# Optimization experiments

Measured on AMD Instinct MI355X. Metric: run time of the kernel, lower is better.

## Reference

```python
import jax, jax.numpy as jnp
import numpy as np

B, N, D = 64, 512, 256
IMG = 51  # hard-coded image-token prefix length from the original forward
EPS = 1e-8


def _l2norm(x):
    # matches torch.cosine_similarity eps clamping on each vector norm
    n = jnp.linalg.norm(x, axis=-1, keepdims=True)
    return x / jnp.maximum(n, EPS)


def setup_inputs() -> dict:
    key = jax.random.key(0)
    ks = jax.random.split(key, 10)
    s = 1.0 / np.sqrt(D)
    return {
        "input_1": jax.random.normal(ks[0], (B, N, D), jnp.float32),
        "input_2": jax.random.normal(ks[1], (B, N, D), jnp.float32),
        "attention_mask": jnp.ones((B, N), jnp.int32),  # unused by forward, kept for signature fidelity
        "noun_mask": jax.random.randint(ks[2], (B, N), 0, 2, jnp.int32),
        "w0": jax.random.uniform(ks[3], (D, D), jnp.float32, -s, s),
        "b0": jax.random.uniform(ks[4], (D,), jnp.float32, -s, s),
        "w1": jax.random.uniform(ks[5], (D, D), jnp.float32, -s, s),
        "b1": jax.random.uniform(ks[6], (D,), jnp.float32, -s, s),
        "wf": jax.random.uniform(ks[7], (D, D), jnp.float32, -s, s),
        "bf": jax.random.uniform(ks[8], (D,), jnp.float32, -s, s),
    }


def reference(input_1, input_2, attention_mask, noun_mask, w0, b0, w1, b1, wf, bf):
    img = _l2norm(input_2[:, :IMG, :])    # [B, 51, D]
    text = _l2norm(input_2[:, IMG:, :])   # [B, N-51, D]
    # cosine similarity via normalized matmul (no O(N*M*D) repeat blowup)
    sim = jnp.einsum('bid,btd->bit', img, text)            # [B, 51, N-51]
    nm = noun_mask[:, IMG:].astype(sim.dtype)[:, None, :]  # [B, 1, N-51]
    sim = sim * nm
    text_sim = jnp.einsum('bid,bjd->bij', text, text)      # [B, N-51, N-51]
    adj = jnp.zeros((B, N, N), input_2.dtype)
    adj = adj.at[:, :IMG, IMG:].set(sim)
    adj = adj.at[:, IMG:, :IMG].set(jnp.swapaxes(sim, 1, 2))
    adj = adj.at[:, IMG:, IMG:].set(text_sim)
    h = input_1
    for w, b in ((w0, b0), (w1, b1)):  # gcn_layer_num = 2; dropout is identity at eval
        h = jax.nn.relu(jnp.einsum('bnm,bmd->bnd', adj, h) @ w.T + b)
    return jax.nn.relu(h @ wf.T + bf)
```

## Files before the change

### kernel.cpp

```cpp
#include <hip/hip_runtime.h>
#include <math.h>

#define Bn   64
#define Nn   512
#define Dn   256
#define IMGn 51

typedef __attribute__((ext_vector_type(8))) short bf16x8;
typedef __attribute__((ext_vector_type(4))) float f32x4;
typedef __attribute__((ext_vector_type(4))) unsigned short u16x4;

__device__ inline unsigned short f2b(float f) {
    union { float f; unsigned u; } v; v.f = f;
    unsigned r = v.u + 0x7fffu + ((v.u >> 16) & 1u);
    return (unsigned short)(r >> 16);
}

__global__ __launch_bounds__(256) void k_prep(const float* __restrict__ in1,
                                              const float* __restrict__ in2,
                                              const float* __restrict__ w0,
                                              const float* __restrict__ w1,
                                              const float* __restrict__ wf,
                                              unsigned short* __restrict__ A0,
                                              unsigned short* __restrict__ T,
                                              unsigned short* __restrict__ w0b,
                                              unsigned short* __restrict__ w1b,
                                              unsigned short* __restrict__ wfb) {
    const int bid = blockIdx.x, tid = threadIdx.x;
    if (bid < 8192) {
        const int row = bid * 4 + (tid >> 6);
        const int lane = tid & 63;
        float4 v = ((const float4*)(in2 + (size_t)row * Dn))[lane];
        float ss = v.x * v.x + v.y * v.y + v.z * v.z + v.w * v.w;
#pragma unroll
        for (int m = 1; m < 64; m <<= 1) ss += __shfl_xor(ss, m);
        float inv = 1.0f / fmaxf(sqrtf(ss), 1e-8f);
        u16x4 o = { f2b(v.x*inv), f2b(v.y*inv), f2b(v.z*inv), f2b(v.w*inv) };
        ((u16x4*)(T + (size_t)row * Dn))[lane] = o;
    } else if (bid < 10240) {
        int i = (bid - 8192) * 256 + tid;
#pragma unroll
        for (int q = 0; q < 4; ++q, i += 524288) {
            float4 v = ((const float4*)in1)[i];
            u16x4 o = { f2b(v.x), f2b(v.y), f2b(v.z), f2b(v.w) };
            ((u16x4*)A0)[i] = o;
        }
    } else {
        const int b2 = bid - 10240;
        const float* src = (b2 < 64) ? w0 : (b2 < 128) ? w1 : wf;
        unsigned short* dst = (b2 < 64) ? w0b : (b2 < 128) ? w1b : wfb;
        const int i = (b2 & 63) * 256 + tid;
        float4 v = ((const float4*)src)[i];
        u16x4 o = { f2b(v.x), f2b(v.y), f2b(v.z), f2b(v.w) };
        ((u16x4*)dst)[i] = o;
    }
}


__device__ inline void stage128x32(const unsigned short* __restrict__ src, int ldk,
                                   char* ldsbase, int tid) {
    const int wave = tid >> 6, lane = tid & 63;
#pragma unroll
    for (int it = 0; it < 2; ++it) {
        const int chunk = wave * 128 + it * 64 + lane;
        const int row = chunk >> 2, s = chunk & 3;
        const char* g = (const char*)(src + (size_t)row * ldk) + ((s ^ ((row >> 1) & 3)) << 4);
        char* l = ldsbase + (size_t)(wave * 2048 + it * 1024);
        __builtin_amdgcn_global_load_lds((const __attribute__((address_space(1))) void*)g,
                                         (__attribute__((address_space(3))) void*)l,
                                         16, 0, 0);
    }
}

__device__ inline bf16x8 frag(const char* ldsbase, int row, int s) {
    return *(const bf16x8*)(ldsbase + row * 64 + ((s ^ ((row >> 1) & 3)) << 4));
}

enum { EPI_GRAM = 0, EPI_TRANS = 1, EPI_BIASH = 2, EPI_FINAL = 3 };

template<int EPI, int NBUF>
__global__ __launch_bounds__(256) void k_mfma(const unsigned short* __restrict__ Abase,
                                              const unsigned short* __restrict__ Bbase,
                                              void* __restrict__ outp,
                                              const float* __restrict__ bias,
                                              const int* __restrict__ noun,
                                              int K, int lda, int ldb, long sA, long sB) {
    extern __shared__ char smem[];
    const int tid = threadIdx.x, lane = tid & 63, wave = tid >> 6;
    const int wr = wave >> 1, wc = wave & 1;
    const int r16 = lane & 15, s = lane >> 4;
    (void)lane;

    const int nwg = gridDim.x * gridDim.y * gridDim.z;
    const int wg  = blockIdx.x + gridDim.x * (blockIdx.y + gridDim.y * blockIdx.z);
    const int swz = (wg & 7) * (nwg >> 3) + (wg >> 3);
    const int tile_x = swz % gridDim.x;
    const int rem    = swz / gridDim.x;
    const int tile_y = rem % gridDim.y;
    const size_t bz  = rem / gridDim.y;

    const unsigned short* A  = Abase + bz * sA + (size_t)tile_y * 128 * lda;
    const unsigned short* Bt = Bbase + bz * sB + (size_t)tile_x * 128 * ldb;

    f32x4 acc[4][4];
#pragma unroll
    for (int m = 0; m < 4; ++m)
#pragma unroll
        for (int n = 0; n < 4; ++n)
            acc[m][n] = (f32x4){0.f, 0.f, 0.f, 0.f};

    const int NT = K >> 5;

    if constexpr (NBUF == 2) {
        stage128x32(A,  lda, smem,        tid);
        stage128x32(Bt, ldb, smem + 8192, tid);
        for (int t = 0; t < NT; ++t) {
            asm volatile("s_waitcnt vmcnt(0)" ::: "memory");
            __builtin_amdgcn_s_barrier();
            __builtin_amdgcn_sched_barrier(0);
            if (t + 1 < NT) {
                char* nb = smem + 16384 * ((t + 1) & 1);
                stage128x32(A  + (t + 1) * 32, lda, nb,        tid);
                stage128x32(Bt + (t + 1) * 32, ldb, nb + 8192, tid);
            }
            __builtin_amdgcn_sched_barrier(0);
            const char* cb = smem + 16384 * (t & 1);
            bf16x8 af[4], bv[4];
#pragma unroll
            for (int m = 0; m < 4; ++m) af[m] = frag(cb, wr * 64 + m * 16 + r16, s);
#pragma unroll
            for (int n = 0; n < 4; ++n) bv[n] = frag(cb + 8192, wc * 64 + n * 16 + r16, s);
#pragma unroll
            for (int m = 0; m < 4; ++m)
#pragma unroll
                for (int n = 0; n < 4; ++n)
                    acc[m][n] = __builtin_amdgcn_mfma_f32_16x16x32_bf16(af[m], bv[n], acc[m][n], 0, 0, 0);
        }
    } else {
        stage128x32(A,       lda, smem,                tid);
        stage128x32(Bt,      ldb, smem + 8192,         tid);
        stage128x32(A + 32,  lda, smem + 16384,        tid);
        stage128x32(Bt + 32, ldb, smem + 16384 + 8192, tid);
        for (int t = 0; t < NT; ++t) {
            if (t < NT - 1) { asm volatile("s_waitcnt vmcnt(4)" ::: "memory"); }
            else            { asm volatile("s_waitcnt vmcnt(0)" ::: "memory"); }
            __builtin_amdgcn_s_barrier();
            __builtin_amdgcn_sched_barrier(0);
            if (t + 2 < NT) {
                char* nb = smem + 16384 * ((t + 2) % 3);
                stage128x32(A  + (t + 2) * 32, lda, nb,        tid);
                stage128x32(Bt + (t + 2) * 32, ldb, nb + 8192, tid);
            }
            __builtin_amdgcn_sched_barrier(0);
            const char* cb = smem + 16384 * (t % 3);
            bf16x8 af[4], bv[4];
#pragma unroll
            for (int m = 0; m < 4; ++m) af[m] = frag(cb, wr * 64 + m * 16 + r16, s);
#pragma unroll
            for (int n = 0; n < 4; ++n) bv[n] = frag(cb + 8192, wc * 64 + n * 16 + r16, s);
#pragma unroll
            for (int m = 0; m < 4; ++m)
#pragma unroll
                for (int n = 0; n < 4; ++n)
                    acc[m][n] = __builtin_amdgcn_mfma_f32_16x16x32_bf16(af[m], bv[n], acc[m][n], 0, 0, 0);
        }
    }
    __syncthreads();

    const int row0 = tile_y * 128, col0 = tile_x * 128;
    unsigned short* lt = (unsigned short*)smem;
    const int row = tid >> 1, h = tid & 1;

    if constexpr (EPI == EPI_GRAM) {
        const int* nm = noun + bz * Nn;
        unsigned short* out = (unsigned short*)outp + bz * ((size_t)Nn * Nn);
#pragma unroll
        for (int n = 0; n < 4; ++n) {
            const int cl = wc * 64 + n * 16 + r16;
            const int c  = col0 + cl;
            const float nmc = (c < IMGn) ? 0.f : (float)nm[c];
#pragma unroll
            for (int m = 0; m < 4; ++m)
#pragma unroll
                for (int i = 0; i < 4; ++i) {
                    const int rl = wr * 64 + m * 16 + s * 4 + i;
                    const int r  = row0 + rl;
                    float mask;
                    if (r < IMGn)      mask = nmc;
                    else if (c < IMGn) mask = (float)nm[r];
                    else               mask = 1.f;
                    lt[rl * 136 + cl] = f2b(acc[m][n][i] * mask);
                }
        }
        __syncthreads();
        const bf16x8* srcv = (const bf16x8*)(lt + (size_t)row * 136 + h * 64);
        bf16x8* dstv = (bf16x8*)(out + (size_t)(row0 + row) * Nn + col0 + h * 64);
#pragma unroll
        for (int q = 0; q < 8; ++q) dstv[q] = srcv[q];
    } else if constexpr (EPI == EPI_BIASH) {
#pragma unroll
        for (int n = 0; n < 4; ++n) {
            const int cl = wc * 64 + n * 16 + r16;
            const float bvv = bias[col0 + cl];
#pragma unroll
            for (int m = 0; m < 4; ++m)
#pragma unroll
                for (int i = 0; i < 4; ++i) {
                    const int rl = wr * 64 + m * 16 + s * 4 + i;
                    lt[rl * 136 + cl] = f2b(fmaxf(acc[m][n][i] + bvv, 0.f));
                }
        }
        __syncthreads();
        unsigned short* out = (unsigned short*)outp + bz * ((size_t)Nn * Dn);
        const bf16x8* srcv = (const bf16x8*)(lt + (size_t)row * 136 + h * 64);
        bf16x8* dstv = (bf16x8*)(out + (size_t)(row0 + row) * Dn + col0 + h * 64);
#pragma unroll
        for (int q = 0; q < 8; ++q) dstv[q] = srcv[q];
    } else if constexpr (EPI == EPI_FINAL) {
        float* lt32 = (float*)smem;
        float* out = (float*)outp;
#pragma unroll
        for (int p = 0; p < 2; ++p) {
            if (p) __syncthreads();
            if (wc == p) {
#pragma unroll
                for (int n = 0; n < 4; ++n) {
                    const int cll = n * 16 + r16;
                    const float bvv = bias[col0 + p * 64 + cll];
#pragma unroll
                    for (int m = 0; m < 4; ++m)
#pragma unroll
                        for (int i = 0; i < 4; ++i) {
                            const int rl = wr * 64 + m * 16 + s * 4 + i;
                            lt32[rl * 68 + cll] = fmaxf(acc[m][n][i] + bvv, 0.f);
                        }
                }
            }
            __syncthreads();
            const float4* srcv = (const float4*)(lt32 + (size_t)row * 68 + h * 32);
            float4* dstv = (float4*)(out + (size_t)(row0 + row) * Dn + col0 + p * 64 + h * 32);
#pragma unroll
            for (int q = 0; q < 8; ++q) dstv[q] = srcv[q];
        }
    } else {
#pragma unroll
        for (int n = 0; n < 4; ++n)
#pragma unroll
            for (int m = 0; m < 4; ++m)
#pragma unroll
                for (int i = 0; i < 4; ++i) {
                    const int ct = wc * 64 + n * 16 + r16;
                    const int rt = wr * 64 + m * 16 + s * 4 + i;
                    lt[ct * 136 + rt] = f2b(acc[m][n][i]);
                }
        __syncthreads();
        const int bm = tile_y;
        const size_t bb = bm >> 2;
        const int rl0 = (bm & 3) * 128;
        unsigned short* out = (unsigned short*)outp + bb * ((size_t)Dn * Nn);
        const int ct = tid >> 1;
        const bf16x8* srcv = (const bf16x8*)(lt + (size_t)ct * 136 + h * 64);
        bf16x8* dstv = (bf16x8*)(out + (size_t)(col0 + ct) * Nn + rl0 + h * 64);
#pragma unroll
        for (int q = 0; q < 8; ++q) dstv[q] = srcv[q];
    }
}

extern "C" void kernel_launch(void* const* d_in, const int* in_sizes, int n_in,
                              void* d_out, int out_size, void* d_ws, size_t ws_size,
                              hipStream_t stream) {
    const float* input_1 = (const float*)d_in[0];
    const float* input_2 = (const float*)d_in[1];
    const int*   noun    = (const int*)d_in[3];
    const float* w0 = (const float*)d_in[4];
    const float* b0 = (const float*)d_in[5];
    const float* w1 = (const float*)d_in[6];
    const float* b1 = (const float*)d_in[7];
    const float* wf = (const float*)d_in[8];
    const float* bf = (const float*)d_in[9];

    unsigned short* ws  = (unsigned short*)d_ws;
    unsigned short* T   = ws;
    unsigned short* A0  = ws + 8388608;
    unsigned short* adj = ws + 16777216;
    unsigned short* Ut  = ws + 33554432;
    unsigned short* H1  = ws + 41943040;
    unsigned short* H2  = ws + 50331648;
    unsigned short* w0b = ws + 58720256;
    unsigned short* w1b = w0b + 65536;
    unsigned short* wfb = w1b + 65536;

    dim3 blk(256);
    k_prep<<<10432, blk, 0, stream>>>(input_1, input_2, w0, w1, wf, A0, T, w0b, w1b, wfb);

    k_mfma<EPI_GRAM, 2><<<dim3(4, 4, Bn), blk, 34816, stream>>>(
        T, T, adj, nullptr, noun, 256, 256, 256, (long)Nn * Dn, (long)Nn * Dn);
    k_mfma<EPI_TRANS, 3><<<dim3(2, 256, 1), blk, 49152, stream>>>(
        A0, w0b, Ut, nullptr, nullptr, 256, 256, 256, 0, 0);
    k_mfma<EPI_BIASH, 3><<<dim3(2, 4, Bn), blk, 49152, stream>>>(
        adj, Ut, H1, b0, nullptr, 512, 512, 512, (long)Nn * Nn, (long)Dn * Nn);
    k_mfma<EPI_TRANS, 3><<<dim3(2, 256, 1), blk, 49152, stream>>>(
        H1, w1b, Ut, nullptr, nullptr, 256, 256, 256, 0, 0);
    k_mfma<EPI_BIASH, 3><<<dim3(2, 4, Bn), blk, 49152, stream>>>(
        adj, Ut, H2, b1, nullptr, 512, 512, 512, (long)Nn * Nn, (long)Dn * Nn);
    k_mfma<EPI_FINAL, 3><<<dim3(2, 256, 1), blk, 49152, stream>>>(
        H2, wfb, d_out, bf, nullptr, 256, 256, 256, 0, 0);
}
```

Measured before the change: 140.5 us.

## Fuse Gram adjacency computation into aggregation matmul, drop materialized adj

The separate Gram kernel that wrote the masked 512x512 bf16 adjacency to global memory is removed. Each aggregation block now recomputes its 128x128 adjacency tile from the normalized features, masks it into LDS, and immediately multiplies it by Ut. This removes the adjacency write and its two reads, but the Gram matmul now runs twice (once per GCN layer) and redundantly per output column tile. The fused kernel also uses a larger static LDS footprint with a 2-stage buffer, which may limit occupancy.

```diff
diff --git a/kernel.cpp b/kernel.cpp
--- a/kernel.cpp
+++ b/kernel.cpp
@@ -56,7 +56,6 @@
     }
 }
 
-
 __device__ inline void stage128x32(const unsigned short* __restrict__ src, int ldk,
                                    char* ldsbase, int tid) {
     const int wave = tid >> 6, lane = tid & 63;
@@ -76,20 +75,162 @@
     return *(const bf16x8*)(ldsbase + row * 64 + ((s ^ ((row >> 1) & 3)) << 4));
 }
 
-enum { EPI_GRAM = 0, EPI_TRANS = 1, EPI_BIASH = 2, EPI_FINAL = 3 };
-
-template<int EPI, int NBUF>
+__global__ __launch_bounds__(256, 2) void k_fused(const unsigned short* __restrict__ T_,
+                                                  const unsigned short* __restrict__ Ut,
+                                                  const float* __restrict__ bias,
+                                                  const int* __restrict__ noun,
+                                                  unsigned short* __restrict__ H) {
+    __shared__ char smem[67584];
+    unsigned short* Sbuf = (unsigned short*)(smem + 32768);
+    const int tid = threadIdx.x, lane = tid & 63, wave = tid >> 6;
+    const int wr = wave >> 1, wc = wave & 1;
+    const int r16 = lane & 15, s = lane >> 4;
+
+    const int nwg = gridDim.x * gridDim.y * gridDim.z;
+    const int wg  = blockIdx.x + gridDim.x * (blockIdx.y + gridDim.y * blockIdx.z);
+    const int swz = (wg & 7) * (nwg >> 3) + (wg >> 3);
+    const int c0  = swz % gridDim.x;
+    const int rem = swz / gridDim.x;
+    const int ty  = rem % gridDim.y;
+    const size_t bz = rem / gridDim.y;
+
+    const unsigned short* Tb = T_ + bz * (size_t)(Nn * Dn);
+    const unsigned short* Ar = Tb + (size_t)ty * 128 * Dn;
+    const unsigned short* Ub = Ut + bz * (size_t)(Dn * Nn) + (size_t)c0 * 128 * Nn;
+    const int* nm = noun + bz * Nn;
+
+    f32x4 acc[4][4];
+#pragma unroll
+    for (int m = 0; m < 4; ++m)
+#pragma unroll
+        for (int n = 0; n < 4; ++n) acc[m][n] = (f32x4){0.f, 0.f, 0.f, 0.f};
+
+    stage128x32(Ar, Dn, smem,        tid);
+    stage128x32(Tb, Dn, smem + 8192, tid);
+    int gs = 0;
+
+    for (int ct = 0; ct < 4; ++ct) {
+        const unsigned short* Bp = Tb + (size_t)ct * 128 * Dn;
+        f32x4 sacc[4][4];
+#pragma unroll
+        for (int m = 0; m < 4; ++m)
+#pragma unroll
+            for (int n = 0; n < 4; ++n) sacc[m][n] = (f32x4){0.f, 0.f, 0.f, 0.f};
+
+        for (int j = 0; j < 8; ++j) {
+            asm volatile("s_waitcnt vmcnt(0)" ::: "memory");
+            __builtin_amdgcn_s_barrier();
+            __builtin_amdgcn_sched_barrier(0);
+            char* nb = smem + 16384 * ((gs + 1) & 1);
+            if (j < 7) {
+                stage128x32(Ar + (j + 1) * 32, Dn, nb,        tid);
+                stage128x32(Bp + (j + 1) * 32, Dn, nb + 8192, tid);
+            } else {
+                stage128x32(Ub + ct * 128,      Nn, nb,        tid);
+                stage128x32(Ub + ct * 128 + 32, Nn, nb + 8192, tid);
+            }
+            __builtin_amdgcn_sched_barrier(0);
+            const char* cb = smem + 16384 * (gs & 1);
+            bf16x8 af[4], bv[4];
+#pragma unroll
+            for (int m = 0; m < 4; ++m) af[m] = frag(cb,        wr * 64 + m * 16 + r16, s);
+#pragma unroll
+            for (int n = 0; n < 4; ++n) bv[n] = frag(cb + 8192, wc * 64 + n * 16 + r16, s);
+#pragma unroll
+            for (int m = 0; m < 4; ++m)
+#pragma unroll
+                for (int n = 0; n < 4; ++n)
+                    sacc[m][n] = __builtin_amdgcn_mfma_f32_16x16x32_bf16(af[m], bv[n], sacc[m][n], 0, 0, 0);
+            ++gs;
+        }
+#pragma unroll
+        for (int n = 0; n < 4; ++n) {
+            const int cl = wc * 64 + n * 16 + r16;
+            const int c  = ct * 128 + cl;
+            const float nmc = (c < IMGn) ? 0.f : (float)nm[c];
+#pragma unroll
+            for (int m = 0; m < 4; ++m)
+#pragma unroll
+                for (int i = 0; i < 4; ++i) {
+                    const int rl = wr * 64 + m * 16 + s * 4 + i;
+                    const int r  = ty * 128 + rl;
+                    float mask;
+                    if (r < IMGn)      mask = nmc;
+                    else if (c < IMGn) mask = (float)nm[r];
+                    else               mask = 1.f;
+                    Sbuf[rl * 136 + cl] = f2b(sacc[m][n][i] * mask);
+                }
+        }
+        __syncthreads();
+
+        for (int u = 0; u < 2; ++u) {
+            asm volatile("s_waitcnt vmcnt(0)" ::: "memory");
+            __builtin_amdgcn_s_barrier();
+            __builtin_amdgcn_sched_barrier(0);
+            char* nb = smem + 16384 * ((gs + 1) & 1);
+            if (u == 0) {
+                stage128x32(Ub + ct * 128 + 64, Nn, nb,        tid);
+                stage128x32(Ub + ct * 128 + 96, Nn, nb + 8192, tid);
+            } else if (ct < 3) {
+                stage128x32(Ar,                      Dn, nb,        tid);
+                stage128x32(Tb + (ct + 1) * 128 * Dn, Dn, nb + 8192, tid);
+            }
+            __builtin_amdgcn_sched_barrier(0);
+            const char* cb = smem + 16384 * (gs & 1);
+#pragma unroll
+            for (int h = 0; h < 2; ++h) {
+                const int kk = u * 2 + h;
+                bf16x8 af[4], bv[4];
+#pragma unroll
+                for (int m = 0; m < 4; ++m)
+                    af[m] = *(const bf16x8*)((const char*)Sbuf +
+                              (size_t)(wr * 64 + m * 16 + r16) * 272 + kk * 64 + s * 16);
+#pragma unroll
+                for (int n = 0; n < 4; ++n) bv[n] = frag(cb + h * 8192, wc * 64 + n * 16 + r16, s);
+#pragma unroll
+                for (int m = 0; m < 4; ++m)
+#pragma unroll
+                    for (int n = 0; n < 4; ++n)
+                        acc[m][n] = __builtin_amdgcn_mfma_f32_16x16x32_bf16(af[m], bv[n], acc[m][n], 0, 0, 0);
+            }
+            ++gs;
+        }
+    }
+
+    __syncthreads();
+#pragma unroll
+    for (int n = 0; n < 4; ++n) {
+        const int cl = wc * 64 + n * 16 + r16;
+        const float bvv = bias[c0 * 128 + cl];
+#pragma unroll
+        for (int m = 0; m < 4; ++m)
+#pragma unroll
+            for (int i = 0; i < 4; ++i) {
+                const int rl = wr * 64 + m * 16 + s * 4 + i;
+                Sbuf[rl * 136 + cl] = f2b(fmaxf(acc[m][n][i] + bvv, 0.f));
+            }
+    }
+    __syncthreads();
+    const int row = tid >> 1, h = tid & 1;
+    unsigned short* out = H + bz * (size_t)(Nn * Dn);
+    const bf16x8* srcv = (const bf16x8*)(Sbuf + (size_t)row * 136 + h * 64);
+    bf16x8* dstv = (bf16x8*)(out + (size_t)(ty * 128 + row) * Dn + c0 * 128 + h * 64);
+#pragma unroll
+    for (int q = 0; q < 8; ++q) dstv[q] = srcv[q];
+}
+
+enum { EPI_TRANS = 1, EPI_FINAL = 3 };
+
+template<int EPI>
 __global__ __launch_bounds__(256) void k_mfma(const unsigned short* __restrict__ Abase,
                                               const unsigned short* __restrict__ Bbase,
                                               void* __restrict__ outp,
                                               const float* __restrict__ bias,
-                                              const int* __restrict__ noun,
-                                              int K, int lda, int ldb, long sA, long sB) {
+                                              int K, int lda, int ldb) {
     extern __shared__ char smem[];
     const int tid = threadIdx.x, lane = tid & 63, wave = tid >> 6;
     const int wr = wave >> 1, wc = wave & 1;
     const int r16 = lane & 15, s = lane >> 4;
-    (void)lane;
 
     const int nwg = gridDim.x * gridDim.y * gridDim.z;
     const int wg  = blockIdx.x + gridDim.x * (blockIdx.y + gridDim.y * blockIdx.z);
@@ -97,73 +238,43 @@
     const int tile_x = swz % gridDim.x;
     const int rem    = swz / gridDim.x;
     const int tile_y = rem % gridDim.y;
-    const size_t bz  = rem / gridDim.y;
-
-    const unsigned short* A  = Abase + bz * sA + (size_t)tile_y * 128 * lda;
-    const unsigned short* Bt = Bbase + bz * sB + (size_t)tile_x * 128 * ldb;
+
+    const unsigned short* A  = Abase + (size_t)tile_y * 128 * lda;
+    const unsigned short* Bt = Bbase + (size_t)tile_x * 128 * ldb;
 
     f32x4 acc[4][4];
 #pragma unroll
     for (int m = 0; m < 4; ++m)
 #pragma unroll
-        for (int n = 0; n < 4; ++n)
-            acc[m][n] = (f32x4){0.f, 0.f, 0.f, 0.f};
+        for (int n = 0; n < 4; ++n) acc[m][n] = (f32x4){0.f, 0.f, 0.f, 0.f};
 
     const int NT = K >> 5;
-
-    if constexpr (NBUF == 2) {
-        stage128x32(A,  lda, smem,        tid);
-        stage128x32(Bt, ldb, smem + 8192, tid);
-        for (int t = 0; t < NT; ++t) {
-            asm volatile("s_waitcnt vmcnt(0)" ::: "memory");
-            __builtin_amdgcn_s_barrier();
-            __builtin_amdgcn_sched_barrier(0);
-            if (t + 1 < NT) {
-                char* nb = smem + 16384 * ((t + 1) & 1);
-                stage128x32(A  + (t + 1) * 32, lda, nb,        tid);
-                stage128x32(Bt + (t + 1) * 32, ldb, nb + 8192, tid);
-            }
-            __builtin_amdgcn_sched_barrier(0);
-            const char* cb = smem + 16384 * (t & 1);
-            bf16x8 af[4], bv[4];
-#pragma unroll
-            for (int m = 0; m < 4; ++m) af[m] = frag(cb, wr * 64 + m * 16 + r16, s);
-#pragma unroll
-            for (int n = 0; n < 4; ++n) bv[n] = frag(cb + 8192, wc * 64 + n * 16 + r16, s);
-#pragma unroll
-            for (int m = 0; m < 4; ++m)
-#pragma unroll
-                for (int n = 0; n < 4; ++n)
-                    acc[m][n] = __builtin_amdgcn_mfma_f32_16x16x32_bf16(af[m], bv[n], acc[m][n], 0, 0, 0);
-        }
-    } else {
-        stage128x32(A,       lda, smem,                tid);
-        stage128x32(Bt,      ldb, smem + 8192,         tid);
-        stage128x32(A + 32,  lda, smem + 16384,        tid);
-        stage128x32(Bt + 32, ldb, smem + 16384 + 8192, tid);
-        for (int t = 0; t < NT; ++t) {
-            if (t < NT - 1) { asm volatile("s_waitcnt vmcnt(4)" ::: "memory"); }
-            else            { asm volatile("s_waitcnt vmcnt(0)" ::: "memory"); }
-            __builtin_amdgcn_s_barrier();
-            __builtin_amdgcn_sched_barrier(0);
-            if (t + 2 < NT) {
-                char* nb = smem + 16384 * ((t + 2) % 3);
-                stage128x32(A  + (t + 2) * 32, lda, nb,        tid);
-                stage128x32(Bt + (t + 2) * 32, ldb, nb + 8192, tid);
-            }
-            __builtin_amdgcn_sched_barrier(0);
-            const char* cb = smem + 16384 * (t % 3);
-            bf16x8 af[4], bv[4];
-#pragma unroll
-            for (int m = 0; m < 4; ++m) af[m] = frag(cb, wr * 64 + m * 16 + r16, s);
-#pragma unroll
-            for (int n = 0; n < 4; ++n) bv[n] = frag(cb + 8192, wc * 64 + n * 16 + r16, s);
-#pragma unroll
-            for (int m = 0; m < 4; ++m)
-#pragma unroll
-                for (int n = 0; n < 4; ++n)
-                    acc[m][n] = __builtin_amdgcn_mfma_f32_16x16x32_bf16(af[m], bv[n], acc[m][n], 0, 0, 0);
-        }
+    stage128x32(A,       lda, smem,                tid);
+    stage128x32(Bt,      ldb, smem + 8192,         tid);
+    stage128x32(A + 32,  lda, smem + 16384,        tid);
+    stage128x32(Bt + 32, ldb, smem + 16384 + 8192, tid);
+    for (int t = 0; t < NT; ++t) {
+        if (t < NT - 1) { asm volatile("s_waitcnt vmcnt(4)" ::: "memory"); }
+        else            { asm volatile("s_waitcnt vmcnt(0)" ::: "memory"); }
+        __builtin_amdgcn_s_barrier();
+        __builtin_amdgcn_sched_barrier(0);
+        if (t + 2 < NT) {
+            char* nb = smem + 16384 * ((t + 2) % 3);
+            stage128x32(A  + (t + 2) * 32, lda, nb,        tid);
+            stage128x32(Bt + (t + 2) * 32, ldb, nb + 8192, tid);
+        }
+        __builtin_amdgcn_sched_barrier(0);
+        const char* cb = smem + 16384 * (t % 3);
+        bf16x8 af[4], bv[4];
+#pragma unroll
+        for (int m = 0; m < 4; ++m) af[m] = frag(cb,        wr * 64 + m * 16 + r16, s);
+#pragma unroll
+        for (int n = 0; n < 4; ++n) bv[n] = frag(cb + 8192, wc * 64 + n * 16 + r16, s);
+#pragma unroll
+        for (int m = 0; m < 4; ++m)
+#pragma unroll
+            for (int n = 0; n < 4; ++n)
+                acc[m][n] = __builtin_amdgcn_mfma_f32_16x16x32_bf16(af[m], bv[n], acc[m][n], 0, 0, 0);
     }
     __syncthreads();
 
@@ -171,52 +282,7 @@
     unsigned short* lt = (unsigned short*)smem;
     const int row = tid >> 1, h = tid & 1;
 
-    if constexpr (EPI == EPI_GRAM) {
-        const int* nm = noun + bz * Nn;
-        unsigned short* out = (unsigned short*)outp + bz * ((size_t)Nn * Nn);
-#pragma unroll
-        for (int n = 0; n < 4; ++n) {
-            const int cl = wc * 64 + n * 16 + r16;
-            const int c  = col0 + cl;
-            const float nmc = (c < IMGn) ? 0.f : (float)nm[c];
-#pragma unroll
-            for (int m = 0; m < 4; ++m)
-#pragma unroll
-                for (int i = 0; i < 4; ++i) {
-                    const int rl = wr * 64 + m * 16 + s * 4 + i;
-                    const int r  = row0 + rl;
-                    float mask;
-                    if (r < IMGn)      mask = nmc;
-                    else if (c < IMGn) mask = (float)nm[r];
-                    else               mask = 1.f;
-                    lt[rl * 136 + cl] = f2b(acc[m][n][i] * mask);
-                }
-        }
-        __syncthreads();
-        const bf16x8* srcv = (const bf16x8*)(lt + (size_t)row * 136 + h * 64);
-        bf16x8* dstv = (bf16x8*)(out + (size_t)(row0 + row) * Nn + col0 + h * 64);
-#pragma unroll
-        for (int q = 0; q < 8; ++q) dstv[q] = srcv[q];
-    } else if constexpr (EPI == EPI_BIASH) {
-#pragma unroll
-        for (int n = 0; n < 4; ++n) {
-            const int cl = wc * 64 + n * 16 + r16;
-            const float bvv = bias[col0 + cl];
-#pragma unroll
-            for (int m = 0; m < 4; ++m)
-#pragma unroll
-                for (int i = 0; i < 4; ++i) {
-                    const int rl = wr * 64 + m * 16 + s * 4 + i;
-                    lt[rl * 136 + cl] = f2b(fmaxf(acc[m][n][i] + bvv, 0.f));
-                }
-        }
-        __syncthreads();
-        unsigned short* out = (unsigned short*)outp + bz * ((size_t)Nn * Dn);
-        const bf16x8* srcv = (const bf16x8*)(lt + (size_t)row * 136 + h * 64);
-        bf16x8* dstv = (bf16x8*)(out + (size_t)(row0 + row) * Dn + col0 + h * 64);
-#pragma unroll
-        for (int q = 0; q < 8; ++q) dstv[q] = srcv[q];
-    } else if constexpr (EPI == EPI_FINAL) {
+    if constexpr (EPI == EPI_FINAL) {
         float* lt32 = (float*)smem;
         float* out = (float*)outp;
 #pragma unroll
@@ -258,9 +324,9 @@
         const size_t bb = bm >> 2;
         const int rl0 = (bm & 3) * 128;
         unsigned short* out = (unsigned short*)outp + bb * ((size_t)Dn * Nn);
-        const int ct = tid >> 1;
-        const bf16x8* srcv = (const bf16x8*)(lt + (size_t)ct * 136 + h * 64);
-        bf16x8* dstv = (bf16x8*)(out + (size_t)(col0 + ct) * Nn + rl0 + h * 64);
+        const int ctc = tid >> 1;
+        const bf16x8* srcv = (const bf16x8*)(lt + (size_t)ctc * 136 + h * 64);
+        bf16x8* dstv = (bf16x8*)(out + (size_t)(col0 + ctc) * Nn + rl0 + h * 64);
 #pragma unroll
         for (int q = 0; q < 8; ++q) dstv[q] = srcv[q];
     }
@@ -281,28 +347,23 @@
 
     unsigned short* ws  = (unsigned short*)d_ws;
     unsigned short* T   = ws;
-    unsigned short* A0  = ws + 8388608;
-    unsigned short* adj = ws + 16777216;
-    unsigned short* Ut  = ws + 33554432;
-    unsigned short* H1  = ws + 41943040;
-    unsigned short* H2  = ws + 50331648;
-    unsigned short* w0b = ws + 58720256;
+    unsigned short* A0  = ws +  8388608;
+    unsigned short* Ut  = ws + 16777216;
+    unsigned short* H1  = ws + 25165824;
+    unsigned short* H2  = ws + 33554432;
+    unsigned short* w0b = ws + 41943040;
     unsigned short* w1b = w0b + 65536;
     unsigned short* wfb = w1b + 65536;
 
     dim3 blk(256);
     k_prep<<<10432, blk, 0, stream>>>(input_1, input_2, w0, w1, wf, A0, T, w0b, w1b, wfb);
 
-    k_mfma<EPI_GRAM, 2><<<dim3(4, 4, Bn), blk, 34816, stream>>>(
-        T, T, adj, nullptr, noun, 256, 256, 256, (long)Nn * Dn, (long)Nn * Dn);
-    k_mfma<EPI_TRANS, 3><<<dim3(2, 256, 1), blk, 49152, stream>>>(
-        A0, w0b, Ut, nullptr, nullptr, 256, 256, 256, 0, 0);
-    k_mfma<EPI_BIASH, 3><<<dim3(2, 4, Bn), blk, 49152, stream>>>(
-        adj, Ut, H1, b0, nullptr, 512, 512, 512, (long)Nn * Nn, (long)Dn * Nn);
-    k_mfma<EPI_TRANS, 3><<<dim3(2, 256, 1), blk, 49152, stream>>>(
-        H1, w1b, Ut, nullptr, nullptr, 256, 256, 256, 0, 0);
-    k_mfma<EPI_BIASH, 3><<<dim3(2, 4, Bn), blk, 49152, stream>>>(
-        adj, Ut, H2, b1, nullptr, 512, 512, 512, (long)Nn * Nn, (long)Dn * Nn);
-    k_mfma<EPI_FINAL, 3><<<dim3(2, 256, 1), blk, 49152, stream>>>(
-        H2, wfb, d_out, bf, nullptr, 256, 256, 256, 0, 0);
-}
+    k_mfma<EPI_TRANS><<<dim3(2, 256, 1), blk, 49152, stream>>>(
+        A0, w0b, Ut, nullptr, 256, 256, 256);
+    k_fused<<<dim3(2, 4, Bn), blk, 0, stream>>>(T, Ut, b0, noun, H1);
+    k_mfma<EPI_TRANS><<<dim3(2, 256, 1), blk, 49152, stream>>>(
+        H1, w1b, Ut, nullptr, 256, 256, 256);
+    k_fused<<<dim3(2, 4, Bn), blk, 0, stream>>>(T, Ut, b1, noun, H2);
+    k_mfma<EPI_FINAL><<<dim3(2, 256, 1), blk, 49152, stream>>>(
+        H2, wfb, d_out, bf, 256, 256, 256);
+}
```

Result: slower. 166.7 us (+18.6%).

## Split GEMM template into per-stage kernels with XCD-aware tile mapping and fusion

Applied to the files above, without the earlier changes.

Replaces the generic templated MFMA kernel with dedicated kernels. Block indices are mapped so that each XCD works on a contiguous set of batches, which is meant to keep per-XCD L2 locality from the prep stage through the following GEMMs. The Gram kernel and the first input-times-weight transform are merged into a single launch to cut one launch and its tail. The GEMM loop drops to plain double buffering with __syncthreads, padded LDS buffers and static 34 KB shared memory with a 4-blocks-per-CU launch bound. The trade-off is a simpler pipeline (loads are no longer staged two ahead), possible extra register pressure, and extra barrier overhead.

```diff
diff --git a/kernel.cpp b/kernel.cpp
--- a/kernel.cpp
+++ b/kernel.cpp
@@ -28,7 +28,9 @@
                                               unsigned short* __restrict__ wfb) {
     const int bid = blockIdx.x, tid = threadIdx.x;
     if (bid < 8192) {
-        const int row = bid * 4 + (tid >> 6);
+        const int xcd = bid & 7, j = bid >> 3;
+        const int b = xcd * 8 + (j >> 7), rb = j & 127;
+        const int row = b * 512 + rb * 4 + (tid >> 6);
         const int lane = tid & 63;
         float4 v = ((const float4*)(in2 + (size_t)row * Dn))[lane];
         float ss = v.x * v.x + v.y * v.y + v.z * v.z + v.w * v.w;
@@ -38,9 +40,12 @@
         u16x4 o = { f2b(v.x*inv), f2b(v.y*inv), f2b(v.z*inv), f2b(v.w*inv) };
         ((u16x4*)(T + (size_t)row * Dn))[lane] = o;
     } else if (bid < 10240) {
-        int i = (bid - 8192) * 256 + tid;
-#pragma unroll
-        for (int q = 0; q < 4; ++q, i += 524288) {
+        const int id2 = bid - 8192;
+        const int xcd = id2 & 7, j = id2 >> 3;
+        const int b = xcd * 8 + (j >> 5), jj = j & 31;
+        int i = b * 32768 + jj * 1024 + tid;
+#pragma unroll
+        for (int q = 0; q < 4; ++q, i += 256) {
             float4 v = ((const float4*)in1)[i];
             u16x4 o = { f2b(v.x), f2b(v.y), f2b(v.z), f2b(v.w) };
             ((u16x4*)A0)[i] = o;
@@ -56,7 +61,6 @@
     }
 }
 
-
 __device__ inline void stage128x32(const unsigned short* __restrict__ src, int ldk,
                                    char* ldsbase, int tid) {
     const int wave = tid >> 6, lane = tid & 63;
@@ -76,104 +80,60 @@
     return *(const bf16x8*)(ldsbase + row * 64 + ((s ^ ((row >> 1) & 3)) << 4));
 }
 
-enum { EPI_GRAM = 0, EPI_TRANS = 1, EPI_BIASH = 2, EPI_FINAL = 3 };
-
-template<int EPI, int NBUF>
-__global__ __launch_bounds__(256) void k_mfma(const unsigned short* __restrict__ Abase,
-                                              const unsigned short* __restrict__ Bbase,
-                                              void* __restrict__ outp,
-                                              const float* __restrict__ bias,
-                                              const int* __restrict__ noun,
-                                              int K, int lda, int ldb, long sA, long sB) {
-    extern __shared__ char smem[];
+__device__ inline void gemm_loop(const unsigned short* __restrict__ A,
+                                 const unsigned short* __restrict__ Bt,
+                                 int lda, int ldb, int NT, char* smem, int tid,
+                                 int wr, int wc, int r16, int s, f32x4 (&acc)[4][4]) {
+#pragma unroll
+    for (int m = 0; m < 4; ++m)
+#pragma unroll
+        for (int n = 0; n < 4; ++n) acc[m][n] = (f32x4){0.f, 0.f, 0.f, 0.f};
+    stage128x32(A,  lda, smem,        tid);
+    stage128x32(Bt, ldb, smem + 8192, tid);
+    __syncthreads();
+    for (int t = 0; t < NT; ++t) {
+        if (t + 1 < NT) {
+            char* nb = smem + 17408 * ((t + 1) & 1);
+            stage128x32(A  + (t + 1) * 32, lda, nb,        tid);
+            stage128x32(Bt + (t + 1) * 32, ldb, nb + 8192, tid);
+        }
+        const char* cb = smem + 17408 * (t & 1);
+        bf16x8 af[4], bv[4];
+#pragma unroll
+        for (int m = 0; m < 4; ++m) af[m] = frag(cb,        wr * 64 + m * 16 + r16, s);
+#pragma unroll
+        for (int n = 0; n < 4; ++n) bv[n] = frag(cb + 8192, wc * 64 + n * 16 + r16, s);
+#pragma unroll
+        for (int m = 0; m < 4; ++m)
+#pragma unroll
+            for (int n = 0; n < 4; ++n)
+                acc[m][n] = __builtin_amdgcn_mfma_f32_16x16x32_bf16(af[m], bv[n], acc[m][n], 0, 0, 0);
+        __syncthreads();
+    }
+}
+
+__global__ __launch_bounds__(256, 4) void k_gt(const unsigned short* __restrict__ T_,
+                                               const unsigned short* __restrict__ A0,
+                                               const unsigned short* __restrict__ w0b,
+                                               const int* __restrict__ noun,
+                                               unsigned short* __restrict__ adj,
+                                               unsigned short* __restrict__ Ut) {
+    __shared__ char smem[34816];
     const int tid = threadIdx.x, lane = tid & 63, wave = tid >> 6;
     const int wr = wave >> 1, wc = wave & 1;
     const int r16 = lane & 15, s = lane >> 4;
-    (void)lane;
-
-    const int nwg = gridDim.x * gridDim.y * gridDim.z;
-    const int wg  = blockIdx.x + gridDim.x * (blockIdx.y + gridDim.y * blockIdx.z);
-    const int swz = (wg & 7) * (nwg >> 3) + (wg >> 3);
-    const int tile_x = swz % gridDim.x;
-    const int rem    = swz / gridDim.x;
-    const int tile_y = rem % gridDim.y;
-    const size_t bz  = rem / gridDim.y;
-
-    const unsigned short* A  = Abase + bz * sA + (size_t)tile_y * 128 * lda;
-    const unsigned short* Bt = Bbase + bz * sB + (size_t)tile_x * 128 * ldb;
-
+    const int id = blockIdx.x, xcd = id & 7, gid = id >> 3;
     f32x4 acc[4][4];
-#pragma unroll
-    for (int m = 0; m < 4; ++m)
-#pragma unroll
-        for (int n = 0; n < 4; ++n)
-            acc[m][n] = (f32x4){0.f, 0.f, 0.f, 0.f};
-
-    const int NT = K >> 5;
-
-    if constexpr (NBUF == 2) {
-        stage128x32(A,  lda, smem,        tid);
-        stage128x32(Bt, ldb, smem + 8192, tid);
-        for (int t = 0; t < NT; ++t) {
-            asm volatile("s_waitcnt vmcnt(0)" ::: "memory");
-            __builtin_amdgcn_s_barrier();
-            __builtin_amdgcn_sched_barrier(0);
-            if (t + 1 < NT) {
-                char* nb = smem + 16384 * ((t + 1) & 1);
-                stage128x32(A  + (t + 1) * 32, lda, nb,        tid);
-                stage128x32(Bt + (t + 1) * 32, ldb, nb + 8192, tid);
-            }
-            __builtin_amdgcn_sched_barrier(0);
-            const char* cb = smem + 16384 * (t & 1);
-            bf16x8 af[4], bv[4];
-#pragma unroll
-            for (int m = 0; m < 4; ++m) af[m] = frag(cb, wr * 64 + m * 16 + r16, s);
-#pragma unroll
-            for (int n = 0; n < 4; ++n) bv[n] = frag(cb + 8192, wc * 64 + n * 16 + r16, s);
-#pragma unroll
-            for (int m = 0; m < 4; ++m)
-#pragma unroll
-                for (int n = 0; n < 4; ++n)
-                    acc[m][n] = __builtin_amdgcn_mfma_f32_16x16x32_bf16(af[m], bv[n], acc[m][n], 0, 0, 0);
-        }
-    } else {
-        stage128x32(A,       lda, smem,                tid);
-        stage128x32(Bt,      ldb, smem + 8192,         tid);
-        stage128x32(A + 32,  lda, smem + 16384,        tid);
-        stage128x32(Bt + 32, ldb, smem + 16384 + 8192, tid);
-        for (int t = 0; t < NT; ++t) {
-            if (t < NT - 1) { asm volatile("s_waitcnt vmcnt(4)" ::: "memory"); }
-            else            { asm volatile("s_waitcnt vmcnt(0)" ::: "memory"); }
-            __builtin_amdgcn_s_barrier();
-            __builtin_amdgcn_sched_barrier(0);
-            if (t + 2 < NT) {
-                char* nb = smem + 16384 * ((t + 2) % 3);
-                stage128x32(A  + (t + 2) * 32, lda, nb,        tid);
-                stage128x32(Bt + (t + 2) * 32, ldb, nb + 8192, tid);
-            }
-            __builtin_amdgcn_sched_barrier(0);
-            const char* cb = smem + 16384 * (t % 3);
-            bf16x8 af[4], bv[4];
-#pragma unroll
-            for (int m = 0; m < 4; ++m) af[m] = frag(cb, wr * 64 + m * 16 + r16, s);
-#pragma unroll
-            for (int n = 0; n < 4; ++n) bv[n] = frag(cb + 8192, wc * 64 + n * 16 + r16, s);
-#pragma unroll
-            for (int m = 0; m < 4; ++m)
-#pragma unroll
-                for (int n = 0; n < 4; ++n)
-                    acc[m][n] = __builtin_amdgcn_mfma_f32_16x16x32_bf16(af[m], bv[n], acc[m][n], 0, 0, 0);
-        }
-    }
-    __syncthreads();
-
-    const int row0 = tile_y * 128, col0 = tile_x * 128;
-    unsigned short* lt = (unsigned short*)smem;
-    const int row = tid >> 1, h = tid & 1;
-
-    if constexpr (EPI == EPI_GRAM) {
-        const int* nm = noun + bz * Nn;
-        unsigned short* out = (unsigned short*)outp + bz * ((size_t)Nn * Nn);
+
+    if (gid < 128) {
+        const int b = xcd * 8 + (gid >> 4);
+        const int tile = gid & 15, bx = tile & 3, by = tile >> 2;
+        const unsigned short* Tb = T_ + (size_t)b * Nn * Dn;
+        gemm_loop(Tb + (size_t)by * 128 * Dn, Tb + (size_t)bx * 128 * Dn,
+                  Dn, Dn, 8, smem, tid, wr, wc, r16, s, acc);
+        const int row0 = by * 128, col0 = bx * 128;
+        const int* nm = noun + b * Nn;
+        unsigned short* lt = (unsigned short*)smem;
 #pragma unroll
         for (int n = 0; n < 4; ++n) {
             const int cl = wc * 64 + n * 16 + r16;
@@ -193,56 +153,18 @@
                 }
         }
         __syncthreads();
+        unsigned short* out = adj + (size_t)b * Nn * Nn;
+        const int row = tid >> 1, h = tid & 1;
         const bf16x8* srcv = (const bf16x8*)(lt + (size_t)row * 136 + h * 64);
         bf16x8* dstv = (bf16x8*)(out + (size_t)(row0 + row) * Nn + col0 + h * 64);
 #pragma unroll
         for (int q = 0; q < 8; ++q) dstv[q] = srcv[q];
-    } else if constexpr (EPI == EPI_BIASH) {
-#pragma unroll
-        for (int n = 0; n < 4; ++n) {
-            const int cl = wc * 64 + n * 16 + r16;
-            const float bvv = bias[col0 + cl];
-#pragma unroll
-            for (int m = 0; m < 4; ++m)
-#pragma unroll
-                for (int i = 0; i < 4; ++i) {
-                    const int rl = wr * 64 + m * 16 + s * 4 + i;
-                    lt[rl * 136 + cl] = f2b(fmaxf(acc[m][n][i] + bvv, 0.f));
-                }
-        }
-        __syncthreads();
-        unsigned short* out = (unsigned short*)outp + bz * ((size_t)Nn * Dn);
-        const bf16x8* srcv = (const bf16x8*)(lt + (size_t)row * 136 + h * 64);
-        bf16x8* dstv = (bf16x8*)(out + (size_t)(row0 + row) * Dn + col0 + h * 64);
-#pragma unroll
-        for (int q = 0; q < 8; ++q) dstv[q] = srcv[q];
-    } else if constexpr (EPI == EPI_FINAL) {
-        float* lt32 = (float*)smem;
-        float* out = (float*)outp;
-#pragma unroll
-        for (int p = 0; p < 2; ++p) {
-            if (p) __syncthreads();
-            if (wc == p) {
-#pragma unroll
-                for (int n = 0; n < 4; ++n) {
-                    const int cll = n * 16 + r16;
-                    const float bvv = bias[col0 + p * 64 + cll];
-#pragma unroll
-                    for (int m = 0; m < 4; ++m)
-#pragma unroll
-                        for (int i = 0; i < 4; ++i) {
-                            const int rl = wr * 64 + m * 16 + s * 4 + i;
-                            lt32[rl * 68 + cll] = fmaxf(acc[m][n][i] + bvv, 0.f);
-                        }
-                }
-            }
-            __syncthreads();
-            const float4* srcv = (const float4*)(lt32 + (size_t)row * 68 + h * 32);
-            float4* dstv = (float4*)(out + (size_t)(row0 + row) * Dn + col0 + p * 64 + h * 32);
-#pragma unroll
-            for (int q = 0; q < 8; ++q) dstv[q] = srcv[q];
-        }
     } else {
+        const int idx = xcd * 64 + (gid - 128);
+        const int tx = idx & 1, ty = idx >> 1;
+        gemm_loop(A0 + (size_t)ty * 128 * Dn, w0b + (size_t)tx * 128 * Dn,
+                  Dn, Dn, 8, smem, tid, wr, wc, r16, s, acc);
+        unsigned short* lt = (unsigned short*)smem;
 #pragma unroll
         for (int n = 0; n < 4; ++n)
 #pragma unroll
@@ -254,13 +176,127 @@
                     lt[ct * 136 + rt] = f2b(acc[m][n][i]);
                 }
         __syncthreads();
-        const int bm = tile_y;
-        const size_t bb = bm >> 2;
-        const int rl0 = (bm & 3) * 128;
-        unsigned short* out = (unsigned short*)outp + bb * ((size_t)Dn * Nn);
-        const int ct = tid >> 1;
+        const size_t bb = ty >> 2;
+        const int rl0 = (ty & 3) * 128, col0 = tx * 128;
+        unsigned short* out = Ut + bb * ((size_t)Dn * Nn);
+        const int ct = tid >> 1, h = tid & 1;
         const bf16x8* srcv = (const bf16x8*)(lt + (size_t)ct * 136 + h * 64);
         bf16x8* dstv = (bf16x8*)(out + (size_t)(col0 + ct) * Nn + rl0 + h * 64);
+#pragma unroll
+        for (int q = 0; q < 8; ++q) dstv[q] = srcv[q];
+    }
+}
+
+__global__ __launch_bounds__(256, 4) void k_biash(const unsigned short* __restrict__ adj,
+                                                  const unsigned short* __restrict__ Ut,
+                                                  const float* __restrict__ bias,
+                                                  unsigned short* __restrict__ H) {
+    __shared__ char smem[34816];
+    const int tid = threadIdx.x, lane = tid & 63, wave = tid >> 6;
+    const int wr = wave >> 1, wc = wave & 1;
+    const int r16 = lane & 15, s = lane >> 4;
+    const int id = blockIdx.x, xcd = id & 7, gid = id >> 3;
+    const int b = xcd * 8 + (gid >> 3);
+    const int tile = gid & 7, tx = tile & 1, ty = tile >> 1;
+    f32x4 acc[4][4];
+    gemm_loop(adj + (size_t)b * Nn * Nn + (size_t)ty * 128 * Nn,
+              Ut  + (size_t)b * Dn * Nn + (size_t)tx * 128 * Nn,
+              Nn, Nn, 16, smem, tid, wr, wc, r16, s, acc);
+    const int row0 = ty * 128, col0 = tx * 128;
+    unsigned short* lt = (unsigned short*)smem;
+#pragma unroll
+    for (int n = 0; n < 4; ++n) {
+        const int cl = wc * 64 + n * 16 + r16;
+        const float bvv = bias[col0 + cl];
+#pragma unroll
+        for (int m = 0; m < 4; ++m)
+#pragma unroll
+            for (int i = 0; i < 4; ++i) {
+                const int rl = wr * 64 + m * 16 + s * 4 + i;
+                lt[rl * 136 + cl] = f2b(fmaxf(acc[m][n][i] + bvv, 0.f));
+            }
+    }
+    __syncthreads();
+    unsigned short* out = H + (size_t)b * Nn * Dn;
+    const int row = tid >> 1, h = tid & 1;
+    const bf16x8* srcv = (const bf16x8*)(lt + (size_t)row * 136 + h * 64);
+    bf16x8* dstv = (bf16x8*)(out + (size_t)(row0 + row) * Dn + col0 + h * 64);
+#pragma unroll
+    for (int q = 0; q < 8; ++q) dstv[q] = srcv[q];
+}
+
+__global__ __launch_bounds__(256, 4) void k_trans(const unsigned short* __restrict__ Hin,
+                                                  const unsigned short* __restrict__ Wb,
+                                                  unsigned short* __restrict__ Ut) {
+    __shared__ char smem[34816];
+    const int tid = threadIdx.x, lane = tid & 63, wave = tid >> 6;
+    const int wr = wave >> 1, wc = wave & 1;
+    const int r16 = lane & 15, s = lane >> 4;
+    const int id = blockIdx.x, xcd = id & 7;
+    const int idx = xcd * 64 + (id >> 3);
+    const int tx = idx & 1, ty = idx >> 1;
+    f32x4 acc[4][4];
+    gemm_loop(Hin + (size_t)ty * 128 * Dn, Wb + (size_t)tx * 128 * Dn,
+              Dn, Dn, 8, smem, tid, wr, wc, r16, s, acc);
+    unsigned short* lt = (unsigned short*)smem;
+#pragma unroll
+    for (int n = 0; n < 4; ++n)
+#pragma unroll
+        for (int m = 0; m < 4; ++m)
+#pragma unroll
+            for (int i = 0; i < 4; ++i) {
+                const int ct = wc * 64 + n * 16 + r16;
+                const int rt = wr * 64 + m * 16 + s * 4 + i;
+                lt[ct * 136 + rt] = f2b(acc[m][n][i]);
+            }
+    __syncthreads();
+    const size_t bb = ty >> 2;
+    const int rl0 = (ty & 3) * 128, col0 = tx * 128;
+    unsigned short* out = Ut + bb * ((size_t)Dn * Nn);
+    const int ct = tid >> 1, h = tid & 1;
+    const bf16x8* srcv = (const bf16x8*)(lt + (size_t)ct * 136 + h * 64);
+    bf16x8* dstv = (bf16x8*)(out + (size_t)(col0 + ct) * Nn + rl0 + h * 64);
+#pragma unroll
+    for (int q = 0; q < 8; ++q) dstv[q] = srcv[q];
+}
+
+__global__ __launch_bounds__(256, 4) void k_final(const unsigned short* __restrict__ H2,
+                                                  const unsigned short* __restrict__ wfb,
+                                                  const float* __restrict__ bias,
+                                                  float* __restrict__ out) {
+    __shared__ char smem[34816];
+    const int tid = threadIdx.x, lane = tid & 63, wave = tid >> 6;
+    const int wr = wave >> 1, wc = wave & 1;
+    const int r16 = lane & 15, s = lane >> 4;
+    const int id = blockIdx.x, xcd = id & 7;
+    const int idx = xcd * 64 + (id >> 3);
+    const int tx = idx & 1, ty = idx >> 1;
+    f32x4 acc[4][4];
+    gemm_loop(H2 + (size_t)ty * 128 * Dn, wfb + (size_t)tx * 128 * Dn,
+              Dn, Dn, 8, smem, tid, wr, wc, r16, s, acc);
+    const int row0 = ty * 128, col0 = tx * 128;
+    float* lt32 = (float*)smem;
+    const int row = tid >> 1, h = tid & 1;
+#pragma unroll
+    for (int p = 0; p < 2; ++p) {
+        if (p) __syncthreads();
+        if (wc == p) {
+#pragma unroll
+            for (int n = 0; n < 4; ++n) {
+                const int cll = n * 16 + r16;
+                const float bvv = bias[col0 + p * 64 + cll];
+#pragma unroll
+                for (int m = 0; m < 4; ++m)
+#pragma unroll
+                    for (int i = 0; i < 4; ++i) {
+                        const int rl = wr * 64 + m * 16 + s * 4 + i;
+                        lt32[rl * 68 + cll] = fmaxf(acc[m][n][i] + bvv, 0.f);
+                    }
+            }
+        }
+        __syncthreads();
+        const float4* srcv = (const float4*)(lt32 + (size_t)row * 68 + h * 32);
+        float4* dstv = (float4*)(out + (size_t)(row0 + row) * Dn + col0 + p * 64 + h * 32);
 #pragma unroll
         for (int q = 0; q < 8; ++q) dstv[q] = srcv[q];
     }
@@ -281,7 +317,7 @@
 
     unsigned short* ws  = (unsigned short*)d_ws;
     unsigned short* T   = ws;
-    unsigned short* A0  = ws + 8388608;
+    unsigned short* A0  = ws +  8388608;
     unsigned short* adj = ws + 16777216;
     unsigned short* Ut  = ws + 33554432;
     unsigned short* H1  = ws + 41943040;
@@ -292,17 +328,9 @@
 
     dim3 blk(256);
     k_prep<<<10432, blk, 0, stream>>>(input_1, input_2, w0, w1, wf, A0, T, w0b, w1b, wfb);
-
-    k_mfma<EPI_GRAM, 2><<<dim3(4, 4, Bn), blk, 34816, stream>>>(
-        T, T, adj, nullptr, noun, 256, 256, 256, (long)Nn * Dn, (long)Nn * Dn);
-    k_mfma<EPI_TRANS, 3><<<dim3(2, 256, 1), blk, 49152, stream>>>(
-        A0, w0b, Ut, nullptr, nullptr, 256, 256, 256, 0, 0);
-    k_mfma<EPI_BIASH, 3><<<dim3(2, 4, Bn), blk, 49152, stream>>>(
-        adj, Ut, H1, b0, nullptr, 512, 512, 512, (long)Nn * Nn, (long)Dn * Nn);
-    k_mfma<EPI_TRANS, 3><<<dim3(2, 256, 1), blk, 49152, stream>>>(
-        H1, w1b, Ut, nullptr, nullptr, 256, 256, 256, 0, 0);
-    k_mfma<EPI_BIASH, 3><<<dim3(2, 4, Bn), blk, 49152, stream>>>(
-        adj, Ut, H2, b1, nullptr, 512, 512, 512, (long)Nn * Nn, (long)Dn * Nn);
-    k_mfma<EPI_FINAL, 3><<<dim3(2, 256, 1), blk, 49152, stream>>>(
-        H2, wfb, d_out, bf, nullptr, 256, 256, 256, 0, 0);
-}
+    k_gt<<<1536, blk, 0, stream>>>(T, A0, w0b, noun, adj, Ut);
+    k_biash<<<512, blk, 0, stream>>>(adj, Ut, b0, H1);
+    k_trans<<<512, blk, 0, stream>>>(H1, w1b, Ut);
+    k_biash<<<512, blk, 0, stream>>>(adj, Ut, b1, H2);
+    k_final<<<512, blk, 0, stream>>>(H2, wfb, bf, (float*)d_out);
+}
```

Result: faster. 128.1 us (-8.8%).
